# Optimization experiments

Measured on AMD Instinct MI355X. Metric: run time of the kernel, lower is better.

The kernel has to match this reference:

```python
import jax, jax.numpy as jnp
import numpy as np

B, IN_CAPS, IN_DIM = 256, 1152, 8
OUT_CAPS, OUT_DIM = 10, 16
NUM_ROUTING = 3


def setup_inputs() -> dict:
    key = jax.random.key(0)
    k_u, k_w = jax.random.split(key)
    u = jax.random.normal(k_u, (B, IN_CAPS, IN_DIM), dtype=jnp.float32)
    # nn.init.normal_(W, mean=0.0, std=0.01); torch shape [1, in, out, out_dim, in_dim]
    W = 0.01 * jax.random.normal(k_w, (IN_CAPS, OUT_CAPS, OUT_DIM, IN_DIM), dtype=jnp.float32)
    return {"u": u, "W": W}


def _squash(s, eps=1e-8):
    # v = (||s||^2 / (1 + ||s||^2)) * s / ||s||, along last dim
    sq = jnp.sum(s * s, axis=-1, keepdims=True)
    return (sq / (1.0 + sq)) * s / jnp.sqrt(sq + eps)


def reference(u, W):
    # u: [b, i, d_in]; W: [i, o, d_out, d_in] -> u_hat: [b, i, o, d_out]
    u_hat = jnp.einsum("iodk,bik->biod", W, u)
    b = jnp.zeros((u.shape[0], IN_CAPS, OUT_CAPS), dtype=u.dtype)
    v = None
    for it in range(NUM_ROUTING):
        c = jax.nn.softmax(b, axis=2)                       # [b, i, o]
        s = jnp.einsum("bio,biod->bod", c, u_hat)           # weighted sum over input caps
        v = _squash(s)                                      # [b, o, d_out]
        if it < NUM_ROUTING - 1:
            b = b + jnp.einsum("biod,bod->bio", u_hat, v)   # agreement
    return v
```

## Files before the change

### kernel.cpp

```cpp
#include <hip/hip_runtime.h>
#include <hip/hip_fp16.h>

#define B_SZ  256
#define IC    1152
#define ID    8
#define OC    10
#define ODIM  16
#define ROWH  160
#define CH    20

__global__ __launch_bounds__(256) void uhat_b_kernel(
    const float* __restrict__ u, const float* __restrict__ W,
    uint4* __restrict__ uhat)
{
    const int i = blockIdx.x;
    const int b = threadIdx.x;

    __shared__ float4 Wl[ROWH * 2];

    const float4* wsrc = (const float4*)(W + (size_t)i * ROWH * ID);
    for (int idx = b; idx < ROWH * 2; idx += 256) Wl[idx] = wsrc[idx];

    const float4* up = (const float4*)(u + ((size_t)b * IC + i) * ID);
    float4 u0 = up[0], u1 = up[1];
    __syncthreads();

    uint4* dst = uhat + ((size_t)b * IC + i) * CH;
    #pragma unroll 4
    for (int c4 = 0; c4 < CH; ++c4) {
        float o[8];
        #pragma unroll
        for (int j = 0; j < 8; ++j) {
            float4 wa = Wl[(c4 * 8 + j) * 2];
            float4 wb = Wl[(c4 * 8 + j) * 2 + 1];
            o[j] = wa.x * u0.x + wa.y * u0.y + wa.z * u0.z + wa.w * u0.w
                 + wb.x * u1.x + wb.y * u1.y + wb.z * u1.z + wb.w * u1.w;
        }
        union { __half2 h2[4]; uint4 q; } pk;
        pk.h2[0] = __floats2half2_rn(o[0], o[1]);
        pk.h2[1] = __floats2half2_rn(o[2], o[3]);
        pk.h2[2] = __floats2half2_rn(o[4], o[5]);
        pk.h2[3] = __floats2half2_rn(o[6], o[7]);
        dst[c4] = pk.q;
    }
}

__global__ __launch_bounds__(1024) void routing3_kernel(
    const uint4* __restrict__ uhat, float* __restrict__ out)
{
    const int b  = blockIdx.x;
    const int t  = threadIdx.x;
    const int wv = t >> 6;
    const int ln = t & 63;
    const int ii = ln >> 4;
    const int os = ln & 15;
    const bool act = (os < OC);
    const int o  = act ? os : (OC - 1);

    __shared__ float sred[16][164];
    __shared__ float vl[ROWH];

    const char* base = (const char*)uhat + (size_t)b * IC * 320 + o * 32;

    float v[16];
    #pragma unroll
    for (int j = 0; j < 16; ++j) v[j] = 0.f;

    const int ibase = wv * 72 + ii;

    for (int p = 0; p < 3; ++p) {
        float s[16];
        #pragma unroll
        for (int j = 0; j < 16; ++j) s[j] = 0.f;

        uint4 A0 = *(const uint4*)(base + (size_t)ibase * 320);
        uint4 A1 = *(const uint4*)(base + (size_t)ibase * 320 + 16);
        uint4 B0 = *(const uint4*)(base + (size_t)(ibase + 4) * 320);
        uint4 B1 = *(const uint4*)(base + (size_t)(ibase + 4) * 320 + 16);

        #pragma unroll 2
        for (int it = 0; it < 18; ++it) {
            uint4 N0 = B0, N1 = B1;
            if (it + 2 < 18) {
                const char* np = base + (size_t)(ibase + (it + 2) * 4) * 320;
                N0 = *(const uint4*)np;
                N1 = *(const uint4*)(np + 16);
            }

            float r[16];
            const __half2* hp0 = (const __half2*)&A0;
            const __half2* hp1 = (const __half2*)&A1;
            #pragma unroll
            for (int q = 0; q < 4; ++q) {
                float2 f = __half22float2(hp0[q]);
                float2 g = __half22float2(hp1[q]);
                r[2 * q]     = f.x; r[2 * q + 1] = f.y;
                r[8 + 2 * q] = g.x; r[9 + 2 * q] = g.y;
            }

            if (p == 0) {
                #pragma unroll
                for (int j = 0; j < 16; ++j) s[j] += r[j];
            } else {
                float a = 0.f;
                #pragma unroll
                for (int j = 0; j < 16; ++j) a += r[j] * v[j];

                float e = act ? __expf(a) : 0.f;
                float Z = e;
                Z += __shfl_xor(Z, 1);
                Z += __shfl_xor(Z, 2);
                Z += __shfl_xor(Z, 4);
                Z += __shfl_xor(Z, 8);
                float cf = __fdividef(e, Z);

                #pragma unroll
                for (int j = 0; j < 16; ++j) s[j] += cf * r[j];
            }

            A0 = B0; A1 = B1; B0 = N0; B1 = N1;
        }

        #pragma unroll
        for (int j = 0; j < 16; ++j) {
            s[j] += __shfl_xor(s[j], 16);
            s[j] += __shfl_xor(s[j], 32);
        }
        if (ln < 16 && act) {
            float4* dst = (float4*)&sred[wv][os * 16];
            dst[0] = make_float4(s[0],  s[1],  s[2],  s[3]);
            dst[1] = make_float4(s[4],  s[5],  s[6],  s[7]);
            dst[2] = make_float4(s[8],  s[9],  s[10], s[11]);
            dst[3] = make_float4(s[12], s[13], s[14], s[15]);
        }
        __syncthreads();

        if (t < ROWH) {
            float S = 0.f;
            #pragma unroll
            for (int w2 = 0; w2 < 16; ++w2) S += sred[w2][t];
            if (p == 0) S *= 0.1f;
            float n2 = S * S;
            n2 += __shfl_xor(n2, 1);
            n2 += __shfl_xor(n2, 2);
            n2 += __shfl_xor(n2, 4);
            n2 += __shfl_xor(n2, 8);
            float sc = (n2 / (1.0f + n2)) * rsqrtf(n2 + 1e-8f);
            vl[t] = S * sc;
        }
        __syncthreads();

        if (p < 2) {
            const float4* vp = (const float4*)&vl[o * 16];
            float4 q0 = vp[0], q1 = vp[1], q2 = vp[2], q3 = vp[3];
            if (p == 0) {
                v[0]=q0.x; v[1]=q0.y; v[2]=q0.z; v[3]=q0.w;
                v[4]=q1.x; v[5]=q1.y; v[6]=q1.z; v[7]=q1.w;
                v[8]=q2.x; v[9]=q2.y; v[10]=q2.z; v[11]=q2.w;
                v[12]=q3.x; v[13]=q3.y; v[14]=q3.z; v[15]=q3.w;
            } else {
                v[0]+=q0.x; v[1]+=q0.y; v[2]+=q0.z; v[3]+=q0.w;
                v[4]+=q1.x; v[5]+=q1.y; v[6]+=q1.z; v[7]+=q1.w;
                v[8]+=q2.x; v[9]+=q2.y; v[10]+=q2.z; v[11]+=q2.w;
                v[12]+=q3.x; v[13]+=q3.y; v[14]+=q3.z; v[15]+=q3.w;
            }
            __syncthreads();
        }
    }

    if (t < 2 * CH) {
        ((float4*)out)[(size_t)b * 2 * CH + t] = ((const float4*)vl)[t];
    }
}

extern "C" void kernel_launch(void* const* d_in, const int* in_sizes, int n_in,
                              void* d_out, int out_size, void* d_ws, size_t ws_size,
                              hipStream_t stream)
{
    const float* u = (const float*)d_in[0];
    const float* W = (const float*)d_in[1];

    uint4* uhat = (uint4*)d_ws;

    uhat_b_kernel<<<IC, 256, 0, stream>>>(u, W, uhat);
    routing3_kernel<<<B_SZ, 1024, 0, stream>>>(uhat, (float*)d_out);
}
```

Before: 144.5 us.

## Store u_hat input-capsule-major and deepen routing prefetch to four stages

The u_hat intermediate is now laid out as [i][b][o] rather than [b][i][o]. In the first kernel, consecutive threads (batches) therefore write contiguous 320-byte rows. Each thread buffers all 20 packed outputs in registers before the stores. The routing kernel changes its addressing to stride by input capsule across the batch dimension and moves from a two-deep to a four-deep fully unrolled register prefetch ring. In exchange, routing reads within a block now jump by large strides, and register pressure rises in both kernels.

Measured after the change: 360.2 us. 149% more time.

```diff
diff --git a/kernel.cpp b/kernel.cpp
--- a/kernel.cpp
+++ b/kernel.cpp
@@ -5,11 +5,10 @@
 #define IC    1152
 #define ID    8
 #define OC    10
-#define ODIM  16
 #define ROWH  160
 #define CH    20
 
-__global__ __launch_bounds__(256) void uhat_b_kernel(
+__global__ __launch_bounds__(256) void uhat_ib_kernel(
     const float* __restrict__ u, const float* __restrict__ W,
     uint4* __restrict__ uhat)
 {
@@ -25,8 +24,8 @@
     float4 u0 = up[0], u1 = up[1];
     __syncthreads();
 
-    uint4* dst = uhat + ((size_t)b * IC + i) * CH;
-    #pragma unroll 4
+    uint4 ro[CH];
+    #pragma unroll
     for (int c4 = 0; c4 < CH; ++c4) {
         float o[8];
         #pragma unroll
@@ -41,8 +40,12 @@
         pk.h2[1] = __floats2half2_rn(o[2], o[3]);
         pk.h2[2] = __floats2half2_rn(o[4], o[5]);
         pk.h2[3] = __floats2half2_rn(o[6], o[7]);
-        dst[c4] = pk.q;
+        ro[c4] = pk.q;
     }
+
+    uint4* dst = uhat + ((size_t)i * B_SZ + b) * CH;
+    #pragma unroll
+    for (int c4 = 0; c4 < CH; ++c4) dst[c4] = ro[c4];
 }
 
 __global__ __launch_bounds__(1024) void routing3_kernel(
@@ -60,31 +63,36 @@
     __shared__ float sred[16][164];
     __shared__ float vl[ROWH];
 
-    const char* base = (const char*)uhat + (size_t)b * IC * 320 + o * 32;
+    const char* base = (const char*)uhat
+                     + ((size_t)(wv * 72 + ii) * B_SZ + b) * 320 + o * 32;
+    const size_t STEP = (size_t)4 * B_SZ * 320;
 
     float v[16];
     #pragma unroll
     for (int j = 0; j < 16; ++j) v[j] = 0.f;
-
-    const int ibase = wv * 72 + ii;
 
     for (int p = 0; p < 3; ++p) {
         float s[16];
         #pragma unroll
         for (int j = 0; j < 16; ++j) s[j] = 0.f;
 
-        uint4 A0 = *(const uint4*)(base + (size_t)ibase * 320);
-        uint4 A1 = *(const uint4*)(base + (size_t)ibase * 320 + 16);
-        uint4 B0 = *(const uint4*)(base + (size_t)(ibase + 4) * 320);
-        uint4 B1 = *(const uint4*)(base + (size_t)(ibase + 4) * 320 + 16);
+        uint4 P[4][2];
+        #pragma unroll
+        for (int k = 0; k < 4; ++k) {
+            const char* ap = base + (size_t)k * STEP;
+            P[k][0] = *(const uint4*)ap;
+            P[k][1] = *(const uint4*)(ap + 16);
+        }
 
-        #pragma unroll 2
+        #pragma unroll
         for (int it = 0; it < 18; ++it) {
-            uint4 N0 = B0, N1 = B1;
-            if (it + 2 < 18) {
-                const char* np = base + (size_t)(ibase + (it + 2) * 4) * 320;
-                N0 = *(const uint4*)np;
-                N1 = *(const uint4*)(np + 16);
+            const int slot = it & 3;
+            uint4 A0 = P[slot][0];
+            uint4 A1 = P[slot][1];
+            if (it + 4 < 18) {
+                const char* np = base + (size_t)(it + 4) * STEP;
+                P[slot][0] = *(const uint4*)np;
+                P[slot][1] = *(const uint4*)(np + 16);
             }
 
             float r[16];
@@ -117,8 +125,6 @@
                 #pragma unroll
                 for (int j = 0; j < 16; ++j) s[j] += cf * r[j];
             }
-
-            A0 = B0; A1 = B1; B0 = N0; B1 = N1;
         }
 
         #pragma unroll
@@ -182,6 +188,6 @@
 
     uint4* uhat = (uint4*)d_ws;
 
-    uhat_b_kernel<<<IC, 256, 0, stream>>>(u, W, uhat);
+    uhat_ib_kernel<<<IC, 256, 0, stream>>>(u, W, uhat);
     routing3_kernel<<<B_SZ, 1024, 0, stream>>>(uhat, (float*)d_out);
 }
```
